# Kernel tuning notes

Hardware: AMD Instinct MI355X
Metric: run time of the kernel (lower is better)

Reference implementation:

```python
import jax, jax.numpy as jnp
import numpy as np

N_NODES = 50000
N_EDGES = 600000
F_IN = 64
N_GRAPHS = 2000
OUT_DIM = 1
BN_EPS = 1e-5


def _bn(x, gamma, beta):
    # BatchNorm1d training-mode forward: biased batch stats over node/row dim
    m = jnp.mean(x, axis=0)
    v = jnp.var(x, axis=0)
    return (x - m) * jax.lax.rsqrt(v + BN_EPS) * gamma + beta


def _gcn(x, W, b, src, dst):
    # PyG GCNConv: h = x @ W; symmetric-normalized aggregation with self-loops; bias after agg
    n = x.shape[0]
    h = x @ W                                    # [N, C_out]
    ones = jnp.ones((src.shape[0],), h.dtype)
    deg = jax.ops.segment_sum(ones, dst, num_segments=n) + 1.0  # +1 self-loop
    dinv = jax.lax.rsqrt(deg)
    norm = (dinv[src] * dinv[dst])[:, None]      # [E, 1]
    agg = jax.ops.segment_sum(h[src] * norm, dst, num_segments=n)
    agg = agg + h * (1.0 / deg)[:, None]         # self-loop term: deg^{-1/2}*deg^{-1/2}
    return agg + b


def _pool_mean(x, batch, g):
    s = jax.ops.segment_sum(x, batch, num_segments=g)
    c = jax.ops.segment_sum(jnp.ones((x.shape[0],), x.dtype), batch, num_segments=g)
    return s / jnp.maximum(c, 1.0)[:, None]


def _forward(xc, xs, W1c, b1c, g1c, be1c, W2c, b2c, g2c, be2c,
             W1s, b1s, g1s, be1s, W2s, b2s, g2s, be2s,
             Wf1, bf1, gf1, bef1, Wf2, bf2,
             src_c, dst_c, src_s, dst_s, batch):
    hc = jax.nn.relu(_bn(_gcn(xc, W1c, b1c, src_c, dst_c), g1c, be1c))
    hc = jax.nn.relu(_bn(_gcn(hc, W2c, b2c, src_c, dst_c), g2c, be2c))
    hs = jax.nn.relu(_bn(_gcn(xs, W1s, b1s, src_s, dst_s), g1s, be1s))
    hs = jax.nn.relu(_bn(_gcn(hs, W2s, b2s, src_s, dst_s), g2s, be2s))
    pc = _pool_mean(hc, batch, N_GRAPHS)         # [G, 64]
    ps = _pool_mean(hs, batch, N_GRAPHS)         # [G, 64]
    h = jnp.concatenate([pc, ps], axis=1)        # [G, 128]
    h = jax.nn.relu(_bn(h @ Wf1 + bf1, gf1, bef1))  # dropout is identity in eval
    return h @ Wf2 + bf2                         # [G, OUT_DIM]


def setup_inputs() -> dict:
    key = jax.random.key(0)
    ks = jax.random.split(key, 16)

    def glorot(k, fan_in, fan_out):
        s = np.sqrt(2.0 / (fan_in + fan_out)).astype(np.float32)
        return jax.random.normal(k, (fan_in, fan_out), jnp.float32) * s

    inp = {
        'x_chromophore': jax.random.normal(ks[0], (N_NODES, F_IN), jnp.float32),
        'x_solvent': jax.random.normal(ks[1], (N_NODES, F_IN), jnp.float32),
        'edge_index_chromophore': jax.random.randint(ks[2], (2, N_EDGES), 0, N_NODES),
        'edge_index_solvent': jax.random.randint(ks[3], (2, N_EDGES), 0, N_NODES),
        'batch': jnp.sort(jax.random.randint(ks[4], (N_NODES,), 0, N_GRAPHS)),
        # chromophore branch params
        'W1c': glorot(ks[5], F_IN, 128), 'b1c': jnp.zeros((128,), jnp.float32),
        'g1c': jnp.ones((128,), jnp.float32), 'be1c': jnp.zeros((128,), jnp.float32),
        'W2c': glorot(ks[6], 128, 64), 'b2c': jnp.zeros((64,), jnp.float32),
        'g2c': jnp.ones((64,), jnp.float32), 'be2c': jnp.zeros((64,), jnp.float32),
        # solvent branch params
        'W1s': glorot(ks[7], F_IN, 128), 'b1s': jnp.zeros((128,), jnp.float32),
        'g1s': jnp.ones((128,), jnp.float32), 'be1s': jnp.zeros((128,), jnp.float32),
        'W2s': glorot(ks[8], 128, 64), 'b2s': jnp.zeros((64,), jnp.float32),
        'g2s': jnp.ones((64,), jnp.float32), 'be2s': jnp.zeros((64,), jnp.float32),
        # MLP head
        'Wf1': glorot(ks[9], 128, 64), 'bf1': jnp.zeros((64,), jnp.float32),
        'gf1': jnp.ones((64,), jnp.float32), 'bef1': jnp.zeros((64,), jnp.float32),
        'Wf2': glorot(ks[10], 64, OUT_DIM), 'bf2': jnp.zeros((OUT_DIM,), jnp.float32),
    }
    return inp


def reference(x_chromophore, x_solvent, edge_index_chromophore, edge_index_solvent, batch,
              W1c, b1c, g1c, be1c, W2c, b2c, g2c, be2c,
              W1s, b1s, g1s, be1s, W2s, b2s, g2s, be2s,
              Wf1, bf1, gf1, bef1, Wf2, bf2):
    src_c, dst_c = edge_index_chromophore[0], edge_index_chromophore[1]
    src_s, dst_s = edge_index_solvent[0], edge_index_solvent[1]
    return _forward(x_chromophore, x_solvent,
                    W1c, b1c, g1c, be1c, W2c, b2c, g2c, be2c,
                    W1s, b1s, g1s, be1s, W2s, b2s, g2s, be2s,
                    Wf1, bf1, gf1, bef1, Wf2, bf2,
                    src_c, dst_c, src_s, dst_s, batch)
```

## Files before the change

kernel.cpp:

```cpp
#include <hip/hip_runtime.h>
#include <hip/hip_bf16.h>
#include <cstdint>
#include <cstddef>

#define NN 50000
#define NE 600000
#define NG 2000
#define NBUCK 49
#define SLOTS 16
#define NCHUNK 3125

typedef __attribute__((ext_vector_type(8))) short bf8;
typedef __attribute__((ext_vector_type(4))) float f32x4;

__device__ __forceinline__ unsigned short f2bf(float f) {
    uint32_t u = __float_as_uint(f);
    uint32_t r = (u + 0x7FFFu + ((u >> 16) & 1u)) >> 16;
    return (unsigned short)r;
}
__device__ __forceinline__ float bf2f(unsigned short h) {
    return __uint_as_float(((uint32_t)h) << 16);
}

__global__ __launch_bounds__(256) void conv_bf16_kernel(const float* __restrict__ x0,
                                                        const float* __restrict__ x1,
                                                        unsigned short* __restrict__ out) {
    int b = blockIdx.y;
    const float* x = b ? x1 : x0;
    unsigned short* o = out + (size_t)b * NN * 64;
    int i = (blockIdx.x * 256 + threadIdx.x) * 4;
    if (i + 3 < NN * 64) {
        float4 v = *(const float4*)&x[i];
        ushort4 r = make_ushort4(f2bf(v.x), f2bf(v.y), f2bf(v.z), f2bf(v.w));
        *(ushort4*)&o[i] = r;
    }
}

template<int K, int N>
__global__ __launch_bounds__(256) void pack_w(const float* __restrict__ W0,
                                              const float* __restrict__ W1,
                                              unsigned short* __restrict__ out) {
    int b = blockIdx.y;
    const float* W = b ? W1 : W0;
    unsigned short* o = out + (size_t)b * K * N;
    int idx = blockIdx.x * 256 + threadIdx.x;
    const int total = (N / 16) * (K / 32) * 64;
    if (idx >= total) return;
    int l = idx & 63;
    int th = idx >> 6;
    int h = th % (K / 32);
    int t = th / (K / 32);
    int col = t * 16 + (l & 15);
    int k0 = h * 32 + (l >> 4) * 8;
    ushort4 lo = make_ushort4(f2bf(W[(k0 + 0) * N + col]), f2bf(W[(k0 + 1) * N + col]),
                              f2bf(W[(k0 + 2) * N + col]), f2bf(W[(k0 + 3) * N + col]));
    ushort4 hi = make_ushort4(f2bf(W[(k0 + 4) * N + col]), f2bf(W[(k0 + 5) * N + col]),
                              f2bf(W[(k0 + 6) * N + col]), f2bf(W[(k0 + 7) * N + col]));
    *(ushort4*)&o[idx * 8] = lo;
    *(ushort4*)&o[idx * 8 + 4] = hi;
}

__global__ __launch_bounds__(256) void bucket_hist(const int* __restrict__ d0,
                                                   const int* __restrict__ d1,
                                                   int* __restrict__ bucketCnt, int nE) {
    int b = blockIdx.y;
    const int* dst = b ? d1 : d0;
    __shared__ int h[NBUCK];
    for (int i = threadIdx.x; i < NBUCK; i += 256) h[i] = 0;
    __syncthreads();
    for (int e = blockIdx.x * 256 + threadIdx.x; e < nE; e += gridDim.x * 256)
        atomicAdd(&h[dst[e] >> 10], 1);
    __syncthreads();
    for (int i = threadIdx.x; i < NBUCK; i += 256)
        if (h[i]) atomicAdd(&bucketCnt[b * NBUCK + i], h[i]);
}

__global__ void bucket_scan(const int* __restrict__ bucketCnt,
                            int* __restrict__ bucketOff, int* __restrict__ bucketCur) {
    int b = threadIdx.x;
    if (b < 2) {
        int run = 0;
        for (int i = 0; i < NBUCK; ++i) {
            bucketOff[b * NBUCK + i] = run;
            bucketCur[b * NBUCK + i] = run;
            run += bucketCnt[b * NBUCK + i];
        }
    }
}

__global__ __launch_bounds__(256) void bucket_scatter(const int* __restrict__ s0,
                                                      const int* __restrict__ d0,
                                                      const int* __restrict__ s1,
                                                      const int* __restrict__ d1,
                                                      int* __restrict__ bucketCur,
                                                      uint32_t* __restrict__ bent, int nE) {
    int b = blockIdx.y;
    const int* src = b ? s1 : s0;
    const int* dst = b ? d1 : d0;
    __shared__ int cnt[NBUCK];
    __shared__ int base[NBUCK];
    const int tid = threadIdx.x;
    for (int i = tid; i < NBUCK; i += 256) cnt[i] = 0;
    __syncthreads();

    const int e0 = blockIdx.x * 2048 + tid;
    int bk[8], slot[8];
    uint32_t pay[8];
#pragma unroll
    for (int k = 0; k < 8; ++k) {
        int e = e0 + k * 256;
        if (e < nE) {
            int d = dst[e], s = src[e];
            bk[k] = d >> 10;
            pay[k] = ((uint32_t)(d & 1023) << 16) | (uint32_t)s;
            slot[k] = atomicAdd(&cnt[bk[k]], 1);
        } else bk[k] = -1;
    }
    __syncthreads();
    for (int i = tid; i < NBUCK; i += 256) {
        int c = cnt[i];
        base[i] = c ? atomicAdd(&bucketCur[b * NBUCK + i], c) : 0;
    }
    __syncthreads();
#pragma unroll
    for (int k = 0; k < 8; ++k)
        if (bk[k] >= 0)
            bent[(size_t)b * NE + base[bk[k]] + slot[k]] = pay[k];
}

__global__ __launch_bounds__(256) void csr_build(const uint32_t* __restrict__ bent,
                                                 const int* __restrict__ bucketOff,
                                                 const int* __restrict__ bucketCnt,
                                                 int* __restrict__ row_ptr,
                                                 float* __restrict__ dinv,
                                                 uint16_t* __restrict__ perm) {
    __shared__ int lcnt[1024];
    __shared__ int lcur[1024];
    __shared__ int sscan[256];
    const int bk = blockIdx.x;
    const int b = blockIdx.y;
    const int tid = threadIdx.x;
    const int ebase = bucketOff[b * NBUCK + bk];
    const int ecnt = bucketCnt[b * NBUCK + bk];
    const int node0 = bk << 10;
    const uint32_t* be = bent + (size_t)b * NE + ebase;
    int* rp = row_ptr + b * (NN + 1);
    float* dv = dinv + (size_t)b * NN;
    uint16_t* pm = perm + (size_t)b * NE + ebase;

    for (int i = tid; i < 1024; i += 256) lcnt[i] = 0;
    __syncthreads();
    for (int i = tid; i < ecnt; i += 256) atomicAdd(&lcnt[be[i] >> 16], 1);
    __syncthreads();

    int c[4], s = 0;
#pragma unroll
    for (int j = 0; j < 4; ++j) { c[j] = lcnt[tid * 4 + j]; s += c[j]; }
    sscan[tid] = s;
    __syncthreads();
    for (int off = 1; off < 256; off <<= 1) {
        int v = (tid >= off) ? sscan[tid - off] : 0;
        __syncthreads();
        sscan[tid] += v;
        __syncthreads();
    }
    int run = sscan[tid] - s;
#pragma unroll
    for (int j = 0; j < 4; ++j) {
        int nl = tid * 4 + j;
        int g = node0 + nl;
        if (g < NN) {
            rp[g] = ebase + run;
            lcur[nl] = run;
            dv[g] = rsqrtf((float)c[j] + 1.0f);
        }
        run += c[j];
    }
    if (bk == NBUCK - 1 && tid == 0) rp[NN] = ebase + ecnt;
    __syncthreads();

    for (int i = tid; i < ecnt; i += 256) {
        uint32_t en = be[i];
        int nl = en >> 16;
        int pos = atomicAdd(&lcur[nl], 1);
        pm[pos] = (uint16_t)(en & 0xFFFFu);
    }
}

__global__ __launch_bounds__(256) void weight_fill(const uint16_t* __restrict__ perm,
                                                   const float* __restrict__ dinv,
                                                   uint32_t* __restrict__ permw, int nE) {
    int b = blockIdx.y;
    const uint16_t* pm = perm + (size_t)b * NE;
    const float* dv = dinv + (size_t)b * NN;
    uint32_t* pw = permw + (size_t)b * NE;
    int i = (blockIdx.x * 256 + threadIdx.x) * 4;
    if (i + 3 < nE) {
        ushort4 s4 = *(const ushort4*)&pm[i];
        uint4 o;
        o.x = ((uint32_t)f2bf(dv[s4.x]) << 16) | (uint32_t)s4.x;
        o.y = ((uint32_t)f2bf(dv[s4.y]) << 16) | (uint32_t)s4.y;
        o.z = ((uint32_t)f2bf(dv[s4.z]) << 16) | (uint32_t)s4.z;
        o.w = ((uint32_t)f2bf(dv[s4.w]) << 16) | (uint32_t)s4.w;
        *(uint4*)&pw[i] = o;
    } else {
        for (; i < nE; ++i) {
            uint16_t s = pm[i];
            pw[i] = ((uint32_t)f2bf(dv[s]) << 16) | (uint32_t)s;
        }
    }
}

template<bool STATS>
__global__ __launch_bounds__(256) void gemm1_mfma(const unsigned short* __restrict__ Xbf,
                                                  const unsigned short* __restrict__ Wp,
                                                  unsigned short* __restrict__ Y,
                                                  float* __restrict__ sums) {
    __shared__ float ls[128], ls2[128];
    const int b = blockIdx.y;
    const unsigned short* __restrict__ X = Xbf + (size_t)b * NN * 64;
    const unsigned short* __restrict__ W = Wp + (size_t)b * 64 * 128;
    unsigned short* __restrict__ Yb = Y + (size_t)b * NN * 128;
    const int tid = threadIdx.x;
    const int w = tid >> 6, lane = tid & 63;
    if (STATS) {
        for (int i = tid; i < 128; i += 256) { ls[i] = 0.f; ls2[i] = 0.f; }
        __syncthreads();
    }
    const int chunk = blockIdx.x * 4 + w;
    const bool act = chunk < NCHUNK;
    const int m = lane & 15, quad = lane >> 4;

    if (act) {
        const int row = chunk * 16 + m;
        bf8 a0 = *(const bf8*)&X[(size_t)row * 64 + quad * 8];
        bf8 a1 = *(const bf8*)&X[(size_t)row * 64 + 32 + quad * 8];
        f32x4 acc[8];
#pragma unroll
        for (int t = 0; t < 8; ++t) acc[t] = (f32x4){0.f, 0.f, 0.f, 0.f};
#pragma unroll
        for (int t = 0; t < 8; ++t) {
            bf8 b0 = *(const bf8*)&W[((t * 2 + 0) * 64 + lane) * 8];
            bf8 b1 = *(const bf8*)&W[((t * 2 + 1) * 64 + lane) * 8];
            acc[t] = __builtin_amdgcn_mfma_f32_16x16x32_bf16(a0, b0, acc[t], 0, 0, 0);
            acc[t] = __builtin_amdgcn_mfma_f32_16x16x32_bf16(a1, b1, acc[t], 0, 0, 0);
        }
        const int rbase = chunk * 16 + quad * 4;
#pragma unroll
        for (int t = 0; t < 8; ++t) {
            float s = 0.f, s2 = 0.f;
#pragma unroll
            for (int r = 0; r < 4; ++r) {
                float v = acc[t][r];
                Yb[(size_t)(rbase + r) * 128 + t * 16 + m] = f2bf(v);
                s += v; s2 = fmaf(v, v, s2);
            }
            if (STATS) {
                atomicAdd(&ls[t * 16 + m], s);
                atomicAdd(&ls2[t * 16 + m], s2);
            }
        }
    }
    if (STATS) {
        __syncthreads();
        int slot = blockIdx.x & (SLOTS - 1);
        float* sb = sums + (size_t)(b * SLOTS + slot) * 256;
        if (tid < 128) {
            atomicAdd(&sb[tid], ls[tid]);
            atomicAdd(&sb[128 + tid], ls2[tid]);
        }
    }
}

__global__ __launch_bounds__(256) void gemm2_mfma(const unsigned short* __restrict__ H1,
                                                  const unsigned short* __restrict__ Wp,
                                                  const float* __restrict__ scale,
                                                  const float* __restrict__ shift,
                                                  unsigned short* __restrict__ Y) {
    const int b = blockIdx.y;
    const unsigned short* __restrict__ X = H1 + (size_t)b * NN * 128;
    const unsigned short* __restrict__ W = Wp + (size_t)b * 128 * 64;
    const float* sc = scale + b * 128;
    const float* sh = shift + b * 128;
    unsigned short* __restrict__ Yb = Y + (size_t)b * NN * 64;
    const int tid = threadIdx.x;
    const int w = tid >> 6, lane = tid & 63;
    const int chunk = blockIdx.x * 4 + w;
    if (chunk >= NCHUNK) return;
    const int m = lane & 15, quad = lane >> 4;
    const int row = chunk * 16 + m;

    f32x4 acc[4];
#pragma unroll
    for (int t = 0; t < 4; ++t) acc[t] = (f32x4){0.f, 0.f, 0.f, 0.f};
#pragma unroll
    for (int h = 0; h < 4; ++h) {
        const int k0 = h * 32 + quad * 8;
        bf8 araw = *(const bf8*)&X[(size_t)row * 128 + k0];
        float4 sc0 = *(const float4*)&sc[k0];
        float4 sc1 = *(const float4*)&sc[k0 + 4];
        float4 sh0 = *(const float4*)&sh[k0];
        float4 sh1 = *(const float4*)&sh[k0 + 4];
        float scv[8] = {sc0.x, sc0.y, sc0.z, sc0.w, sc1.x, sc1.y, sc1.z, sc1.w};
        float shv[8] = {sh0.x, sh0.y, sh0.z, sh0.w, sh1.x, sh1.y, sh1.z, sh1.w};
        bf8 af;
#pragma unroll
        for (int j = 0; j < 8; ++j) {
            float v = bf2f((unsigned short)araw[j]);
            v = fmaxf(fmaf(v, scv[j], shv[j]), 0.f);
            af[j] = (short)f2bf(v);
        }
#pragma unroll
        for (int t = 0; t < 4; ++t) {
            bf8 bf = *(const bf8*)&W[((t * 4 + h) * 64 + lane) * 8];
            acc[t] = __builtin_amdgcn_mfma_f32_16x16x32_bf16(af, bf, acc[t], 0, 0, 0);
        }
    }
    const int rbase = chunk * 16 + quad * 4;
#pragma unroll
    for (int t = 0; t < 4; ++t)
#pragma unroll
        for (int r = 0; r < 4; ++r)
            Yb[(size_t)(rbase + r) * 64 + t * 16 + m] = f2bf(acc[t][r]);
}

template<bool STATS>
__global__ __launch_bounds__(256) void agg2_kernel(const unsigned short* __restrict__ hall,
                                                   const int* __restrict__ row_ptr,
                                                   const uint32_t* __restrict__ permw,
                                                   const float* __restrict__ dinv,
                                                   unsigned short* __restrict__ out,
                                                   float* __restrict__ sums, int nNodes) {
    const int b = blockIdx.y;
    const unsigned short* __restrict__ h = hall + (size_t)b * NN * 64;
    const int* rp = row_ptr + b * (NN + 1);
    const uint32_t* pe = permw + (size_t)b * NE;
    const float* dv = dinv + (size_t)b * NN;
    unsigned short* ob = out + (size_t)b * nNodes * 64;

    const int w = threadIdx.x >> 6;
    const int wave = blockIdx.x * 4 + w;
    const int lane = threadIdx.x & 63;
    const int q = lane & 15;
    const int r = lane >> 4;
    float f0 = 0.f, f1 = 0.f, f2 = 0.f, f3 = 0.f;
    const bool active = wave < nNodes;
    if (active) {
        const int d = wave;
        const float di = dv[d];
        const int p0 = rp[d], p1 = rp[d + 1];
        float a0 = 0.f, a1 = 0.f, a2 = 0.f, a3 = 0.f;
        for (int p = p0; p < p1; p += 16) {
            uint32_t en[4];
#pragma unroll
            for (int k = 0; k < 4; ++k) {
                int e = p + k * 4 + r;
                bool vld = e < p1;
                en[k] = pe[vld ? e : p0];
                if (!vld) en[k] &= 0xFFFFu;
            }
#pragma unroll
            for (int k = 0; k < 4; ++k) {
                const int idx = (int)(en[k] & 0xFFFFu);
                const float wk = __uint_as_float(en[k] & 0xFFFF0000u);
                const uint2 hv = *(const uint2*)&h[(size_t)idx * 64 + q * 4];
                a0 = fmaf(wk, __uint_as_float(hv.x << 16), a0);
                a1 = fmaf(wk, __uint_as_float(hv.x & 0xFFFF0000u), a1);
                a2 = fmaf(wk, __uint_as_float(hv.y << 16), a2);
                a3 = fmaf(wk, __uint_as_float(hv.y & 0xFFFF0000u), a3);
            }
        }
        a0 += __shfl_xor(a0, 16, 64); a0 += __shfl_xor(a0, 32, 64);
        a1 += __shfl_xor(a1, 16, 64); a1 += __shfl_xor(a1, 32, 64);
        a2 += __shfl_xor(a2, 16, 64); a2 += __shfl_xor(a2, 32, 64);
        a3 += __shfl_xor(a3, 16, 64); a3 += __shfl_xor(a3, 32, 64);
        const uint2 sv = *(const uint2*)&h[(size_t)d * 64 + q * 4];
        f0 = di * fmaf(di, __uint_as_float(sv.x << 16), a0);
        f1 = di * fmaf(di, __uint_as_float(sv.x & 0xFFFF0000u), a1);
        f2 = di * fmaf(di, __uint_as_float(sv.y << 16), a2);
        f3 = di * fmaf(di, __uint_as_float(sv.y & 0xFFFF0000u), a3);
        if (r == 0) {
            uint32_t o0 = (uint32_t)f2bf(f0) | ((uint32_t)f2bf(f1) << 16);
            uint32_t o1 = (uint32_t)f2bf(f2) | ((uint32_t)f2bf(f3) << 16);
            *(uint2*)&ob[(size_t)d * 64 + q * 4] = make_uint2(o0, o1);
        }
    }
    if constexpr (STATS) {
        __shared__ float ls[256], ls2[256];
        if (lane < 16) {
            *(float4*)&ls[w * 64 + q * 4]  = make_float4(f0, f1, f2, f3);
            *(float4*)&ls2[w * 64 + q * 4] = make_float4(f0 * f0, f1 * f1, f2 * f2, f3 * f3);
        }
        __syncthreads();
        if (threadIdx.x < 64) {
            const int t = threadIdx.x;
            float s  = ls[t]  + ls[t + 64]  + ls[t + 128]  + ls[t + 192];
            float s2 = ls2[t] + ls2[t + 64] + ls2[t + 128] + ls2[t + 192];
            int slot = blockIdx.x & (SLOTS - 1);
            float* sb = sums + ((size_t)(b * SLOTS + slot) * 2) * 64;
            atomicAdd(&sb[t], s);
            atomicAdd(&sb[64 + t], s2);
        }
    }
}

__global__ void bn_finalize2_kernel(const float* __restrict__ sums, int C, float invN,
                                    const float* __restrict__ g0, const float* __restrict__ g1,
                                    const float* __restrict__ b0, const float* __restrict__ b1,
                                    float* __restrict__ scale, float* __restrict__ shift) {
    int b = blockIdx.y;
    int c = threadIdx.x;
    if (c >= C) return;
    float s = 0.f, s2 = 0.f;
    for (int k = 0; k < SLOTS; ++k) {
        const float* sb = sums + ((size_t)(b * SLOTS + k) * 2) * C;
        s += sb[c];
        s2 += sb[C + c];
    }
    const float* gamma = b ? g1 : g0;
    const float* beta = b ? b1 : b0;
    float m = s * invN;
    float var = s2 * invN - m * m;
    float sc = gamma[c] * rsqrtf(var + 1e-5f);
    scale[b * C + c] = sc;
    shift[b * C + c] = beta[c] - m * sc;
}

__global__ void bn_finalize_kernel(const float* __restrict__ sums, int C, float invN,
                                   const float* __restrict__ gamma, const float* __restrict__ beta,
                                   float* __restrict__ scale, float* __restrict__ shift) {
    int c = blockIdx.x * blockDim.x + threadIdx.x;
    if (c >= C) return;
    float m = sums[c] * invN;
    float var = sums[C + c] * invN - m * m;
    float sc = gamma[c] * rsqrtf(var + 1e-5f);
    scale[c] = sc;
    shift[c] = beta[c] - m * sc;
}

__global__ __launch_bounds__(64) void pool2_kernel(const unsigned short* __restrict__ x,
                                                   const float* __restrict__ scale,
                                                   const float* __restrict__ shift,
                                                   const int* __restrict__ batch,
                                                   float* __restrict__ Hmean, int n) {
    int b = blockIdx.y;
    const unsigned short* xb = x + (size_t)b * NN * 64;
    int g = blockIdx.x;
    int c = threadIdx.x;
    int lo = 0, hi = n;
    while (lo < hi) { int mid = (lo + hi) >> 1; if (batch[mid] < g) lo = mid + 1; else hi = mid; }
    int start = lo;
    hi = n;
    while (lo < hi) { int mid = (lo + hi) >> 1; if (batch[mid] <= g) lo = mid + 1; else hi = mid; }
    int end = lo;
    float s = 0.f;
    float sc = scale[b * 64 + c], sh = shift[b * 64 + c];
    for (int r = start; r < end; ++r)
        s += fmaxf(fmaf(bf2f(xb[(size_t)r * 64 + c]), sc, sh), 0.f);
    float cf = (float)(end - start);
    Hmean[(size_t)g * 128 + b * 64 + c] = s / fmaxf(cf, 1.f);
}

__global__ __launch_bounds__(64) void head_gemm1_kernel(const float* __restrict__ H,
                                                        const float* __restrict__ Wf1,
                                                        float* __restrict__ T) {
    __shared__ float row[128];
    int g = blockIdx.x;
    int c = threadIdx.x;
    row[c] = H[(size_t)g * 128 + c];
    row[c + 64] = H[(size_t)g * 128 + 64 + c];
    __syncthreads();
    float acc = 0.f;
#pragma unroll 8
    for (int k = 0; k < 128; ++k) acc = fmaf(row[k], Wf1[k * 64 + c], acc);
    T[(size_t)g * 64 + c] = acc;
}

__global__ __launch_bounds__(64) void head_final_kernel(const float* __restrict__ T,
                                                        const float* __restrict__ scale,
                                                        const float* __restrict__ shift,
                                                        const float* __restrict__ Wf2,
                                                        const float* __restrict__ bf2,
                                                        float* __restrict__ out) {
    int g = blockIdx.x;
    int c = threadIdx.x;
    float v = fmaxf(fmaf(T[(size_t)g * 64 + c], scale[c], shift[c]), 0.f) * Wf2[c];
#pragma unroll
    for (int off = 32; off > 0; off >>= 1) v += __shfl_down(v, off, 64);
    if (c == 0) out[g] = v + bf2[0];
}

template<int C>
__global__ __launch_bounds__(256) void bn_stats_kernel(const float* __restrict__ x, int n,
                                                       float* __restrict__ sums) {
    constexpr int RP = 256 / C;
    __shared__ float ls[256], ls2[256];
    int c = threadIdx.x % C;
    int sub = threadIdx.x / C;
    float s = 0.f, s2 = 0.f;
    for (int r = blockIdx.x * RP + sub; r < n; r += gridDim.x * RP) {
        float v = x[(size_t)r * C + c];
        s += v; s2 += v * v;
    }
    ls[threadIdx.x] = s; ls2[threadIdx.x] = s2;
    __syncthreads();
    if (sub == 0) {
#pragma unroll
        for (int k = 1; k < RP; ++k) { s += ls[k * C + c]; s2 += ls2[k * C + c]; }
        atomicAdd(&sums[c], s);
        atomicAdd(&sums[C + c], s2);
    }
}


static inline size_t alignup(size_t x) { return (x + 255) & ~(size_t)255; }

extern "C" void kernel_launch(void* const* d_in, const int* in_sizes, int n_in,
                              void* d_out, int out_size, void* d_ws, size_t ws_size,
                              hipStream_t stream) {
    const float* xc  = (const float*)d_in[0];
    const float* xs  = (const float*)d_in[1];
    const int*   eic = (const int*)d_in[2];
    const int*   eis = (const int*)d_in[3];
    const int*   batch = (const int*)d_in[4];
    const float* W1c = (const float*)d_in[5];
    const float* g1c = (const float*)d_in[7];
    const float* be1c = (const float*)d_in[8];
    const float* W2c = (const float*)d_in[9];
    const float* g2c = (const float*)d_in[11];
    const float* be2c = (const float*)d_in[12];
    const float* W1s = (const float*)d_in[13];
    const float* g1s = (const float*)d_in[15];
    const float* be1s = (const float*)d_in[16];
    const float* W2s = (const float*)d_in[17];
    const float* g2s = (const float*)d_in[19];
    const float* be2s = (const float*)d_in[20];
    const float* Wf1 = (const float*)d_in[21];
    const float* gf1 = (const float*)d_in[23];
    const float* bef1 = (const float*)d_in[24];
    const float* Wf2 = (const float*)d_in[25];
    const float* bf2 = (const float*)d_in[26];
    float* out = (float*)d_out;

    char* ws = (char*)d_ws;
    size_t off = 0;
    auto alloc = [&](size_t bytes) { char* p = ws + off; off += alignup(bytes); return p; };

    int*      bucketCnt = (int*)alloc(2 * NBUCK * 4);
    int*      bucketOff = (int*)alloc(2 * NBUCK * 4);
    int*      bucketCur = (int*)alloc(2 * NBUCK * 4);
    uint32_t* bent      = (uint32_t*)alloc((size_t)2 * NE * 4);
    uint16_t* perm      = (uint16_t*)alloc(((size_t)2 * NE + 64) * 2);
    int*      row_ptr   = (int*)alloc(2 * (NN + 1) * 4);
    float*    dinv      = (float*)alloc((size_t)2 * NN * 4);
    unsigned short* xbf   = (unsigned short*)alloc((size_t)2 * NN * 64 * 2);
    unsigned short* aggbf = (unsigned short*)alloc((size_t)2 * NN * 64 * 2);
    unsigned short* h1bf  = (unsigned short*)alloc((size_t)2 * NN * 128 * 2);
    unsigned short* h2bf  = (unsigned short*)alloc((size_t)2 * NN * 64 * 2);
    unsigned short* Wp1   = (unsigned short*)alloc((size_t)2 * 64 * 128 * 2);
    unsigned short* Wp2   = (unsigned short*)alloc((size_t)2 * 128 * 64 * 2);
    float*    sums1     = (float*)alloc(((size_t)2 * SLOTS * 256 + (size_t)2 * SLOTS * 128 + 128) * 4);
    float*    sums2     = sums1 + (size_t)2 * SLOTS * 256;
    float*    hsums     = sums2 + (size_t)2 * SLOTS * 128;
    float*    bnscale   = (float*)alloc(2 * 128 * 4);
    float*    bnshift   = (float*)alloc(2 * 128 * 4);
    float*    Hmean     = (float*)alloc((size_t)NG * 128 * 4);
    float*    T         = (float*)alloc((size_t)NG * 64 * 4);

    const float invN = 1.0f / (float)NN;
    const size_t statBytes = ((size_t)2 * SLOTS * 256 + (size_t)2 * SLOTS * 128 + 128) * 4;
    const int gemmBlocks = (NCHUNK + 3) / 4;
    const int aggBlocks = (NN + 3) / 4;

    conv_bf16_kernel<<<dim3((NN * 64 / 4 + 255) / 256, 2), 256, 0, stream>>>(xc, xs, xbf);
    pack_w<64, 128><<<dim3(4, 2), 256, 0, stream>>>(W1c, W1s, Wp1);
    pack_w<128, 64><<<dim3(4, 2), 256, 0, stream>>>(W2c, W2s, Wp2);
    hipMemsetAsync(sums1, 0, statBytes, stream);

    hipMemsetAsync(bucketCnt, 0, 2 * NBUCK * 4, stream);
    bucket_hist<<<dim3(64, 2), 256, 0, stream>>>(eic + NE, eis + NE, bucketCnt, NE);
    bucket_scan<<<1, 64, 0, stream>>>(bucketCnt, bucketOff, bucketCur);
    bucket_scatter<<<dim3((NE + 2047) / 2048, 2), 256, 0, stream>>>(
        eic, eic + NE, eis, eis + NE, bucketCur, bent, NE);
    csr_build<<<dim3(NBUCK, 2), 256, 0, stream>>>(bent, bucketOff, bucketCnt,
                                                  row_ptr, dinv, perm);
    weight_fill<<<dim3((NE / 4 + 255) / 256, 2), 256, 0, stream>>>(perm, dinv, bent, NE);

    agg2_kernel<false><<<dim3(aggBlocks, 2), 256, 0, stream>>>(
        xbf, row_ptr, bent, dinv, aggbf, nullptr, NN);
    gemm1_mfma<true><<<dim3(gemmBlocks, 2), 256, 0, stream>>>(aggbf, Wp1, h1bf, sums1);
    bn_finalize2_kernel<<<dim3(1, 2), 128, 0, stream>>>(sums1, 128, invN,
                                                        g1c, g1s, be1c, be1s, bnscale, bnshift);

    gemm2_mfma<<<dim3(gemmBlocks, 2), 256, 0, stream>>>(h1bf, Wp2, bnscale, bnshift, h2bf);
    agg2_kernel<true><<<dim3(aggBlocks, 2), 256, 0, stream>>>(
        h2bf, row_ptr, bent, dinv, aggbf, sums2, NN);
    bn_finalize2_kernel<<<dim3(1, 2), 64, 0, stream>>>(sums2, 64, invN,
                                                       g2c, g2s, be2c, be2s, bnscale, bnshift);

    pool2_kernel<<<dim3(NG, 2), 64, 0, stream>>>(aggbf, bnscale, bnshift, batch, Hmean, NN);

    head_gemm1_kernel<<<NG, 64, 0, stream>>>(Hmean, Wf1, T);
    bn_stats_kernel<64><<<32, 256, 0, stream>>>(T, NG, hsums);
    bn_finalize_kernel<<<1, 64, 0, stream>>>(hsums, 64, 1.0f / (float)NG, gf1, bef1,
                                             bnscale, bnshift);
    head_final_kernel<<<NG, 64, 0, stream>>>(T, bnscale, bnshift, Wf2, bf2, out);
}
```

Before: 382.9 us.

## Fold BN finalize into consumers, split gemm1 stats, vectorize MFMA output stores

Removes the three separate BN finalize launches by recomputing scale and shift inside gemm2, pool2 and head_final from the slot sums. gemm1 loses its fused shared-memory atomic statistics and gains swapped MFMA operands, so each lane holds four consecutive columns of one row and writes them as a packed 8-byte store. A new stats128_bf16 kernel re-reads h1 from memory to compute the column statistics. This trades fewer launches and coalesced stores against an extra pass over the 128-wide intermediate, and the statistics are now taken from bf16-rounded values.

```diff
diff --git a/kernel.cpp b/kernel.cpp
--- a/kernel.cpp
+++ b/kernel.cpp
@@ -211,79 +211,108 @@
     }
 }
 
-template<bool STATS>
 __global__ __launch_bounds__(256) void gemm1_mfma(const unsigned short* __restrict__ Xbf,
                                                   const unsigned short* __restrict__ Wp,
-                                                  unsigned short* __restrict__ Y,
-                                                  float* __restrict__ sums) {
-    __shared__ float ls[128], ls2[128];
+                                                  unsigned short* __restrict__ Y) {
     const int b = blockIdx.y;
     const unsigned short* __restrict__ X = Xbf + (size_t)b * NN * 64;
     const unsigned short* __restrict__ W = Wp + (size_t)b * 64 * 128;
     unsigned short* __restrict__ Yb = Y + (size_t)b * NN * 128;
     const int tid = threadIdx.x;
     const int w = tid >> 6, lane = tid & 63;
-    if (STATS) {
-        for (int i = tid; i < 128; i += 256) { ls[i] = 0.f; ls2[i] = 0.f; }
-        __syncthreads();
-    }
     const int chunk = blockIdx.x * 4 + w;
-    const bool act = chunk < NCHUNK;
+    if (chunk >= NCHUNK) return;
     const int m = lane & 15, quad = lane >> 4;
 
-    if (act) {
-        const int row = chunk * 16 + m;
-        bf8 a0 = *(const bf8*)&X[(size_t)row * 64 + quad * 8];
-        bf8 a1 = *(const bf8*)&X[(size_t)row * 64 + 32 + quad * 8];
-        f32x4 acc[8];
-#pragma unroll
-        for (int t = 0; t < 8; ++t) acc[t] = (f32x4){0.f, 0.f, 0.f, 0.f};
-#pragma unroll
-        for (int t = 0; t < 8; ++t) {
-            bf8 b0 = *(const bf8*)&W[((t * 2 + 0) * 64 + lane) * 8];
-            bf8 b1 = *(const bf8*)&W[((t * 2 + 1) * 64 + lane) * 8];
-            acc[t] = __builtin_amdgcn_mfma_f32_16x16x32_bf16(a0, b0, acc[t], 0, 0, 0);
-            acc[t] = __builtin_amdgcn_mfma_f32_16x16x32_bf16(a1, b1, acc[t], 0, 0, 0);
-        }
-        const int rbase = chunk * 16 + quad * 4;
-#pragma unroll
-        for (int t = 0; t < 8; ++t) {
-            float s = 0.f, s2 = 0.f;
-#pragma unroll
-            for (int r = 0; r < 4; ++r) {
-                float v = acc[t][r];
-                Yb[(size_t)(rbase + r) * 128 + t * 16 + m] = f2bf(v);
-                s += v; s2 = fmaf(v, v, s2);
-            }
-            if (STATS) {
-                atomicAdd(&ls[t * 16 + m], s);
-                atomicAdd(&ls2[t * 16 + m], s2);
-            }
-        }
-    }
-    if (STATS) {
-        __syncthreads();
+    const int row = chunk * 16 + m;
+    bf8 a0 = *(const bf8*)&X[(size_t)row * 64 + quad * 8];
+    bf8 a1 = *(const bf8*)&X[(size_t)row * 64 + 32 + quad * 8];
+    f32x4 acc[8];
+#pragma unroll
+    for (int t = 0; t < 8; ++t) acc[t] = (f32x4){0.f, 0.f, 0.f, 0.f};
+#pragma unroll
+    for (int t = 0; t < 8; ++t) {
+        bf8 b0 = *(const bf8*)&W[((t * 2 + 0) * 64 + lane) * 8];
+        bf8 b1 = *(const bf8*)&W[((t * 2 + 1) * 64 + lane) * 8];
+        acc[t] = __builtin_amdgcn_mfma_f32_16x16x32_bf16(b0, a0, acc[t], 0, 0, 0);
+        acc[t] = __builtin_amdgcn_mfma_f32_16x16x32_bf16(b1, a1, acc[t], 0, 0, 0);
+    }
+#pragma unroll
+    for (int t = 0; t < 8; ++t) {
+        uint32_t lo = (uint32_t)f2bf(acc[t][0]) | ((uint32_t)f2bf(acc[t][1]) << 16);
+        uint32_t hi = (uint32_t)f2bf(acc[t][2]) | ((uint32_t)f2bf(acc[t][3]) << 16);
+        *(uint2*)&Yb[(size_t)row * 128 + t * 16 + quad * 4] = make_uint2(lo, hi);
+    }
+}
+
+__global__ __launch_bounds__(256) void stats128_bf16(const unsigned short* __restrict__ Y,
+                                                     float* __restrict__ sums) {
+    const int b = blockIdx.y;
+    const unsigned short* __restrict__ Yb = Y + (size_t)b * NN * 128;
+    const int g = threadIdx.x & 31;
+    const int rs = threadIdx.x >> 5;
+    float s0 = 0.f, s1 = 0.f, s2 = 0.f, s3 = 0.f;
+    float q0 = 0.f, q1 = 0.f, q2 = 0.f, q3 = 0.f;
+    for (int r = blockIdx.x * 8 + rs; r < NN; r += gridDim.x * 8) {
+        uint2 v = *(const uint2*)&Yb[(size_t)r * 128 + g * 4];
+        float x0 = __uint_as_float(v.x << 16);
+        float x1 = __uint_as_float(v.x & 0xFFFF0000u);
+        float x2 = __uint_as_float(v.y << 16);
+        float x3 = __uint_as_float(v.y & 0xFFFF0000u);
+        s0 += x0; s1 += x1; s2 += x2; s3 += x3;
+        q0 = fmaf(x0, x0, q0); q1 = fmaf(x1, x1, q1);
+        q2 = fmaf(x2, x2, q2); q3 = fmaf(x3, x3, q3);
+    }
+    __shared__ float ls[8][128], lq[8][128];
+    *(float4*)&ls[rs][g * 4] = make_float4(s0, s1, s2, s3);
+    *(float4*)&lq[rs][g * 4] = make_float4(q0, q1, q2, q3);
+    __syncthreads();
+    if (threadIdx.x < 128) {
+        const int c = threadIdx.x;
+        float S = 0.f, Q = 0.f;
+#pragma unroll
+        for (int k = 0; k < 8; ++k) { S += ls[k][c]; Q += lq[k][c]; }
         int slot = blockIdx.x & (SLOTS - 1);
         float* sb = sums + (size_t)(b * SLOTS + slot) * 256;
-        if (tid < 128) {
-            atomicAdd(&sb[tid], ls[tid]);
-            atomicAdd(&sb[128 + tid], ls2[tid]);
-        }
+        atomicAdd(&sb[c], S);
+        atomicAdd(&sb[128 + c], Q);
     }
 }
 
 __global__ __launch_bounds__(256) void gemm2_mfma(const unsigned short* __restrict__ H1,
                                                   const unsigned short* __restrict__ Wp,
-                                                  const float* __restrict__ scale,
-                                                  const float* __restrict__ shift,
+                                                  const float* __restrict__ sums,
+                                                  const float* __restrict__ g0,
+                                                  const float* __restrict__ g1,
+                                                  const float* __restrict__ be0,
+                                                  const float* __restrict__ be1,
                                                   unsigned short* __restrict__ Y) {
+    __shared__ float scLds[128], shLds[128];
     const int b = blockIdx.y;
     const unsigned short* __restrict__ X = H1 + (size_t)b * NN * 128;
     const unsigned short* __restrict__ W = Wp + (size_t)b * 128 * 64;
-    const float* sc = scale + b * 128;
-    const float* sh = shift + b * 128;
     unsigned short* __restrict__ Yb = Y + (size_t)b * NN * 64;
     const int tid = threadIdx.x;
+
+    if (tid < 128) {
+        float s = 0.f, s2 = 0.f;
+#pragma unroll
+        for (int k = 0; k < SLOTS; ++k) {
+            const float* sb = sums + (size_t)(b * SLOTS + k) * 256;
+            s += sb[tid];
+            s2 += sb[128 + tid];
+        }
+        const float invN = 1.0f / (float)NN;
+        float mean = s * invN;
+        float var = s2 * invN - mean * mean;
+        float gamma = b ? g1[tid] : g0[tid];
+        float beta = b ? be1[tid] : be0[tid];
+        float sc = gamma * rsqrtf(var + 1e-5f);
+        scLds[tid] = sc;
+        shLds[tid] = beta - mean * sc;
+    }
+    __syncthreads();
+
     const int w = tid >> 6, lane = tid & 63;
     const int chunk = blockIdx.x * 4 + w;
     if (chunk >= NCHUNK) return;
@@ -297,10 +326,10 @@
     for (int h = 0; h < 4; ++h) {
         const int k0 = h * 32 + quad * 8;
         bf8 araw = *(const bf8*)&X[(size_t)row * 128 + k0];
-        float4 sc0 = *(const float4*)&sc[k0];
-        float4 sc1 = *(const float4*)&sc[k0 + 4];
-        float4 sh0 = *(const float4*)&sh[k0];
-        float4 sh1 = *(const float4*)&sh[k0 + 4];
+        float4 sc0 = *(const float4*)&scLds[k0];
+        float4 sc1 = *(const float4*)&scLds[k0 + 4];
+        float4 sh0 = *(const float4*)&shLds[k0];
+        float4 sh1 = *(const float4*)&shLds[k0 + 4];
         float scv[8] = {sc0.x, sc0.y, sc0.z, sc0.w, sc1.x, sc1.y, sc1.z, sc1.w};
         float shv[8] = {sh0.x, sh0.y, sh0.z, sh0.w, sh1.x, sh1.y, sh1.z, sh1.w};
         bf8 af;
@@ -313,15 +342,15 @@
 #pragma unroll
         for (int t = 0; t < 4; ++t) {
             bf8 bf = *(const bf8*)&W[((t * 4 + h) * 64 + lane) * 8];
-            acc[t] = __builtin_amdgcn_mfma_f32_16x16x32_bf16(af, bf, acc[t], 0, 0, 0);
-        }
-    }
-    const int rbase = chunk * 16 + quad * 4;
-#pragma unroll
-    for (int t = 0; t < 4; ++t)
-#pragma unroll
-        for (int r = 0; r < 4; ++r)
-            Yb[(size_t)(rbase + r) * 64 + t * 16 + m] = f2bf(acc[t][r]);
+            acc[t] = __builtin_amdgcn_mfma_f32_16x16x32_bf16(bf, af, acc[t], 0, 0, 0);
+        }
+    }
+#pragma unroll
+    for (int t = 0; t < 4; ++t) {
+        uint32_t lo = (uint32_t)f2bf(acc[t][0]) | ((uint32_t)f2bf(acc[t][1]) << 16);
+        uint32_t hi = (uint32_t)f2bf(acc[t][2]) | ((uint32_t)f2bf(acc[t][3]) << 16);
+        *(uint2*)&Yb[(size_t)row * 64 + t * 16 + quad * 4] = make_uint2(lo, hi);
+    }
 }
 
 template<bool STATS>
@@ -404,49 +433,33 @@
     }
 }
 
-__global__ void bn_finalize2_kernel(const float* __restrict__ sums, int C, float invN,
-                                    const float* __restrict__ g0, const float* __restrict__ g1,
-                                    const float* __restrict__ b0, const float* __restrict__ b1,
-                                    float* __restrict__ scale, float* __restrict__ shift) {
-    int b = blockIdx.y;
-    int c = threadIdx.x;
-    if (c >= C) return;
-    float s = 0.f, s2 = 0.f;
-    for (int k = 0; k < SLOTS; ++k) {
-        const float* sb = sums + ((size_t)(b * SLOTS + k) * 2) * C;
-        s += sb[c];
-        s2 += sb[C + c];
-    }
-    const float* gamma = b ? g1 : g0;
-    const float* beta = b ? b1 : b0;
-    float m = s * invN;
-    float var = s2 * invN - m * m;
-    float sc = gamma[c] * rsqrtf(var + 1e-5f);
-    scale[b * C + c] = sc;
-    shift[b * C + c] = beta[c] - m * sc;
-}
-
-__global__ void bn_finalize_kernel(const float* __restrict__ sums, int C, float invN,
-                                   const float* __restrict__ gamma, const float* __restrict__ beta,
-                                   float* __restrict__ scale, float* __restrict__ shift) {
-    int c = blockIdx.x * blockDim.x + threadIdx.x;
-    if (c >= C) return;
-    float m = sums[c] * invN;
-    float var = sums[C + c] * invN - m * m;
-    float sc = gamma[c] * rsqrtf(var + 1e-5f);
-    scale[c] = sc;
-    shift[c] = beta[c] - m * sc;
-}
-
 __global__ __launch_bounds__(64) void pool2_kernel(const unsigned short* __restrict__ x,
-                                                   const float* __restrict__ scale,
-                                                   const float* __restrict__ shift,
+                                                   const float* __restrict__ sums,
+                                                   const float* __restrict__ g0,
+                                                   const float* __restrict__ g1,
+                                                   const float* __restrict__ be0,
+                                                   const float* __restrict__ be1,
                                                    const int* __restrict__ batch,
                                                    float* __restrict__ Hmean, int n) {
     int b = blockIdx.y;
     const unsigned short* xb = x + (size_t)b * NN * 64;
     int g = blockIdx.x;
     int c = threadIdx.x;
+    float s0 = 0.f, s20 = 0.f;
+#pragma unroll
+    for (int k = 0; k < SLOTS; ++k) {
+        const float* sb = sums + ((size_t)(b * SLOTS + k) * 2) * 64;
+        s0 += sb[c];
+        s20 += sb[64 + c];
+    }
+    const float invN = 1.0f / (float)NN;
+    float mean = s0 * invN;
+    float var = s20 * invN - mean * mean;
+    float gamma = b ? g1[c] : g0[c];
+    float beta = b ? be1[c] : be0[c];
+    float sc = gamma * rsqrtf(var + 1e-5f);
+    float sh = beta - mean * sc;
+
     int lo = 0, hi = n;
     while (lo < hi) { int mid = (lo + hi) >> 1; if (batch[mid] < g) lo = mid + 1; else hi = mid; }
     int start = lo;
@@ -454,7 +467,6 @@
     while (lo < hi) { int mid = (lo + hi) >> 1; if (batch[mid] <= g) lo = mid + 1; else hi = mid; }
     int end = lo;
     float s = 0.f;
-    float sc = scale[b * 64 + c], sh = shift[b * 64 + c];
     for (int r = start; r < end; ++r)
         s += fmaxf(fmaf(bf2f(xb[(size_t)r * 64 + c]), sc, sh), 0.f);
     float cf = (float)(end - start);
@@ -474,20 +486,6 @@
 #pragma unroll 8
     for (int k = 0; k < 128; ++k) acc = fmaf(row[k], Wf1[k * 64 + c], acc);
     T[(size_t)g * 64 + c] = acc;
-}
-
-__global__ __launch_bounds__(64) void head_final_kernel(const float* __restrict__ T,
-                                                        const float* __restrict__ scale,
-                                                        const float* __restrict__ shift,
-                                                        const float* __restrict__ Wf2,
-                                                        const float* __restrict__ bf2,
-                                                        float* __restrict__ out) {
-    int g = blockIdx.x;
-    int c = threadIdx.x;
-    float v = fmaxf(fmaf(T[(size_t)g * 64 + c], scale[c], shift[c]), 0.f) * Wf2[c];
-#pragma unroll
-    for (int off = 32; off > 0; off >>= 1) v += __shfl_down(v, off, 64);
-    if (c == 0) out[g] = v + bf2[0];
 }
 
 template<int C>
@@ -510,6 +508,26 @@
         atomicAdd(&sums[c], s);
         atomicAdd(&sums[C + c], s2);
     }
+}
+
+__global__ __launch_bounds__(64) void head_final_kernel(const float* __restrict__ T,
+                                                        const float* __restrict__ hsums,
+                                                        const float* __restrict__ gf1,
+                                                        const float* __restrict__ bef1,
+                                                        const float* __restrict__ Wf2,
+                                                        const float* __restrict__ bf2,
+                                                        float* __restrict__ out) {
+    int g = blockIdx.x;
+    int c = threadIdx.x;
+    const float invG = 1.0f / (float)NG;
+    float mean = hsums[c] * invG;
+    float var = hsums[64 + c] * invG - mean * mean;
+    float sc = gf1[c] * rsqrtf(var + 1e-5f);
+    float sh = bef1[c] - mean * sc;
+    float v = fmaxf(fmaf(T[(size_t)g * 64 + c], sc, sh), 0.f) * Wf2[c];
+#pragma unroll
+    for (int off = 32; off > 0; off >>= 1) v += __shfl_down(v, off, 64);
+    if (c == 0) out[g] = v + bf2[0];
 }
 
 
@@ -562,12 +580,9 @@
     float*    sums1     = (float*)alloc(((size_t)2 * SLOTS * 256 + (size_t)2 * SLOTS * 128 + 128) * 4);
     float*    sums2     = sums1 + (size_t)2 * SLOTS * 256;
     float*    hsums     = sums2 + (size_t)2 * SLOTS * 128;
-    float*    bnscale   = (float*)alloc(2 * 128 * 4);
-    float*    bnshift   = (float*)alloc(2 * 128 * 4);
     float*    Hmean     = (float*)alloc((size_t)NG * 128 * 4);
     float*    T         = (float*)alloc((size_t)NG * 64 * 4);
 
-    const float invN = 1.0f / (float)NN;
     const size_t statBytes = ((size_t)2 * SLOTS * 256 + (size_t)2 * SLOTS * 128 + 128) * 4;
     const int gemmBlocks = (NCHUNK + 3) / 4;
     const int aggBlocks = (NN + 3) / 4;
@@ -588,21 +603,18 @@
 
     agg2_kernel<false><<<dim3(aggBlocks, 2), 256, 0, stream>>>(
         xbf, row_ptr, bent, dinv, aggbf, nullptr, NN);
-    gemm1_mfma<true><<<dim3(gemmBlocks, 2), 256, 0, stream>>>(aggbf, Wp1, h1bf, sums1);
-    bn_finalize2_kernel<<<dim3(1, 2), 128, 0, stream>>>(sums1, 128, invN,
-                                                        g1c, g1s, be1c, be1s, bnscale, bnshift);
-
-    gemm2_mfma<<<dim3(gemmBlocks, 2), 256, 0, stream>>>(h1bf, Wp2, bnscale, bnshift, h2bf);
+    gemm1_mfma<<<dim3(gemmBlocks, 2), 256, 0, stream>>>(aggbf, Wp1, h1bf);
+    stats128_bf16<<<dim3(256, 2), 256, 0, stream>>>(h1bf, sums1);
+
+    gemm2_mfma<<<dim3(gemmBlocks, 2), 256, 0, stream>>>(h1bf, Wp2, sums1,
+                                                        g1c, g1s, be1c, be1s, h2bf);
     agg2_kernel<true><<<dim3(aggBlocks, 2), 256, 0, stream>>>(
         h2bf, row_ptr, bent, dinv, aggbf, sums2, NN);
-    bn_finalize2_kernel<<<dim3(1, 2), 64, 0, stream>>>(sums2, 64, invN,
-                                                       g2c, g2s, be2c, be2s, bnscale, bnshift);
-
-    pool2_kernel<<<dim3(NG, 2), 64, 0, stream>>>(aggbf, bnscale, bnshift, batch, Hmean, NN);
+
+    pool2_kernel<<<dim3(NG, 2), 64, 0, stream>>>(aggbf, sums2, g2c, g2s, be2c, be2s,
+                                                 batch, Hmean, NN);
 
     head_gemm1_kernel<<<NG, 64, 0, stream>>>(Hmean, Wf1, T);
     bn_stats_kernel<64><<<32, 256, 0, stream>>>(T, NG, hsums);
-    bn_finalize_kernel<<<1, 64, 0, stream>>>(hsums, 64, 1.0f / (float)NG, gf1, bef1,
-                                             bnscale, bnshift);
-    head_final_kernel<<<NG, 64, 0, stream>>>(T, bnscale, bnshift, Wf2, bf2, out);
-}
+    head_final_kernel<<<NG, 64, 0, stream>>>(T, hsums, gf1, bef1, Wf2, bf2, out);
+}
```

Measured after the change: 354.6 us. 1.08x faster.
